# Performance work log

Measured on AMD Instinct MI355X. Metric: run time of the kernel, lower is better.

Reference implementation:

```python
import jax, jax.numpy as jnp
import numpy as np

N_HEAD = 16
HEAD_SIZE = 1024
EMBED = 1024
MULTI_HEAD_SIZE = HEAD_SIZE // N_HEAD  # 64; used only as the softmax scale (source bug)
B, S = 4, 2048


def setup_inputs() -> dict:
    key = jax.random.key(0)
    k1, k2, k3, k4 = jax.random.split(key, 4)
    x = jax.random.normal(k1, (B, S, EMBED), dtype=jnp.float32)
    w_qkv = jax.random.normal(k2, (3 * HEAD_SIZE, EMBED), dtype=jnp.float32) * 0.02
    w_proj = jax.random.normal(k3, (EMBED, HEAD_SIZE), dtype=jnp.float32) * 0.02
    b_proj = jax.random.normal(k4, (EMBED,), dtype=jnp.float32) * 0.02
    return {"x": x, "w_qkv": w_qkv, "w_proj": w_proj, "b_proj": b_proj}


def reference(x, w_qkv, w_proj, b_proj):
    # Fused QKV projection (Linear, no bias): [B,S,E] @ [E,3H] -> split
    qkv = jnp.einsum("bse,he->bsh", x, w_qkv)  # [B,S,3H]
    q, k, v = jnp.split(qkv, 3, axis=-1)       # each [B,S,H]
    # Source's non-flash path: attention over FULL Head_size dim (not per-head),
    # scaled by sqrt(multi_head_size) -- reproduced faithfully.
    scale = 1.0 / np.sqrt(MULTI_HEAD_SIZE).astype(np.float32)
    scores = jnp.einsum("bqh,bkh->bqk", q, k) * scale  # [B,S,S]
    probs = jax.nn.softmax(scores, axis=-1)            # dropout = identity (eval)
    out = jnp.einsum("bqk,bkh->bqh", probs, v)         # [B,S,H]
    # Faithful scrambling reshape: transpose(1,2).contiguous().view(B,S,H)
    Bn, Sn, H = out.shape
    out = jnp.swapaxes(out, 1, 2).reshape(Bn, Sn, H)
    # Output projection + residual dropout (identity in eval)
    out = jnp.einsum("bsh,eh->bse", out, w_proj) + b_proj
    return out
```

## Files before the change

kernel.cpp:

```cpp
#include <hip/hip_runtime.h>


typedef float f32x4 __attribute__((ext_vector_type(4)));
typedef short bf16x8 __attribute__((ext_vector_type(8)));
typedef short bf16x4 __attribute__((ext_vector_type(4)));
typedef unsigned short u16;

#define BM 128
#define BN 128
#define BK 32

__device__ inline u16 f2bf(float f) {
  union { float f; unsigned u; } x; x.f = f;
  unsigned r = x.u + 0x7fffu + ((x.u >> 16) & 1u);
  return (u16)(r >> 16);
}

__device__ inline void gload_lds16(const void* g, void* l) {
  __builtin_amdgcn_global_load_lds(
      (const __attribute__((address_space(1))) void*)g,
      (__attribute__((address_space(3))) void*)l, 16, 0, 0);
}

__global__ __launch_bounds__(256) void cvt_kernel(const float* __restrict__ in,
                                                  u16* __restrict__ out, int n8) {
  int i = blockIdx.x * 256 + threadIdx.x;
  if (i >= n8) return;
  f32x4 a = *(const f32x4*)&in[(long)i * 8];
  f32x4 b = *(const f32x4*)&in[(long)i * 8 + 4];
  bf16x8 o;
#pragma unroll
  for (int j = 0; j < 4; ++j) { o[j] = (short)f2bf(a[j]); o[4 + j] = (short)f2bf(b[j]); }
  *(bf16x8*)&out[(long)i * 8] = o;
}

__global__ __launch_bounds__(256) void transpose_v(const u16* __restrict__ qkvb,
                                                   u16* __restrict__ vT) {
  __shared__ u16 tile[64][72];
  const int t = threadIdx.x;
  const long b = blockIdx.z;
  const int k0 = blockIdx.x * 64, h0 = blockIdx.y * 64;
  const u16* v = qkvb + b * 2048 * 3072 + 2048;
#pragma unroll
  for (int i = 0; i < 2; ++i) {
    int s = i * 256 + t; int r = s >> 3, c = (s & 7) * 8;
    bf16x8 val = *(const bf16x8*)&v[(long)(k0 + r) * 3072 + h0 + c];
    *(bf16x8*)&tile[r][c] = val;
  }
  __syncthreads();
  u16* o = vT + b * 1024 * 2048;
#pragma unroll
  for (int i = 0; i < 2; ++i) {
    int s = i * 256 + t; int r = s >> 3, c = (s & 7) * 8;
    bf16x8 val;
#pragma unroll
    for (int j = 0; j < 8; ++j) val[j] = tile[c + j][r];
    *(bf16x8*)&o[(long)(h0 + r) * 2048 + k0 + c] = val;
  }
}

__global__ __launch_bounds__(256) void softmax_k(const float* __restrict__ S,
                                                 u16* __restrict__ P,
                                                 long sS, long sP) {
  const int t = threadIdx.x;
  const float* row = S + (long)blockIdx.z * sS + (long)blockIdx.x * 2048;
  u16* prow = P + (long)blockIdx.z * sP + (long)blockIdx.x * 2048;
  f32x4 v0 = *(const f32x4*)&row[t * 8];
  f32x4 v1 = *(const f32x4*)&row[t * 8 + 4];
  float m = v0[0];
#pragma unroll
  for (int j = 1; j < 4; ++j) m = fmaxf(m, v0[j]);
#pragma unroll
  for (int j = 0; j < 4; ++j) m = fmaxf(m, v1[j]);
#pragma unroll
  for (int o = 32; o; o >>= 1) m = fmaxf(m, __shfl_xor(m, o));
  __shared__ float red[8];
  if ((t & 63) == 0) red[t >> 6] = m;
  __syncthreads();
  m = fmaxf(fmaxf(red[0], red[1]), fmaxf(red[2], red[3]));
  const float C = 0.18033688011112042f;
  float e[8], s = 0.f;
#pragma unroll
  for (int j = 0; j < 4; ++j) { e[j] = exp2f((v0[j] - m) * C); s += e[j]; }
#pragma unroll
  for (int j = 0; j < 4; ++j) { e[4 + j] = exp2f((v1[j] - m) * C); s += e[4 + j]; }
#pragma unroll
  for (int o = 32; o; o >>= 1) s += __shfl_xor(s, o);
  if ((t & 63) == 0) red[4 + (t >> 6)] = s;
  __syncthreads();
  float inv = 1.f / (red[4] + red[5] + red[6] + red[7]);
  bf16x8 ov;
#pragma unroll
  for (int j = 0; j < 8; ++j) ov[j] = (short)f2bf(e[j] * inv);
  *(bf16x8*)&prow[t * 8] = ov;
}

template <int MODE>
__global__ __launch_bounds__(256) void gemm_nt(const u16* __restrict__ A0, int lda, long sAz,
                                               const u16* __restrict__ B0, int ldb, long sBz,
                                               void* __restrict__ C0, int ldc, long sCz,
                                               const float* __restrict__ bias, int K) {
  __shared__ u16 As[2][BM * BK];
  __shared__ u16 Bs[2][BM * BK];
  const int t = threadIdx.x;
  const int lane = t & 63, wv = t >> 6;
  const long row0 = (long)blockIdx.y * BM, col0 = (long)blockIdx.x * BN;
  const u16* A = A0 + (long)blockIdx.z * sAz;
  const u16* B = B0 + (long)blockIdx.z * sBz;

  f32x4 acc[4][4];
#pragma unroll
  for (int m = 0; m < 4; ++m)
#pragma unroll
    for (int n = 0; n < 4; ++n) acc[m][n] = (f32x4){0.f, 0.f, 0.f, 0.f};

  const int wrow = (wv >> 1) * 64, wcol = (wv & 1) * 64;
  const int fr = lane & 15, fk = (lane >> 4) * 8;

  auto stage = [&](int buf, int k0) {
#pragma unroll
    for (int i = 0; i < 2; ++i) {
      int c = i * 256 + wv * 64 + lane;
      int r = c >> 2, sl = c & 3;
      gload_lds16(A + (row0 + r) * lda + k0 + sl * 8, &As[buf][(i * 256 + wv * 64) * 8]);
    }
#pragma unroll
    for (int i = 0; i < 2; ++i) {
      int c = i * 256 + wv * 64 + lane;
      int r = c >> 2, sl = c & 3;
      gload_lds16(B + (col0 + r) * ldb + k0 + sl * 8, &Bs[buf][(i * 256 + wv * 64) * 8]);
    }
  };

  stage(0, 0);
  __syncthreads();
  const int NK = K / BK;
  for (int kt = 0; kt < NK; ++kt) {
    const int cur = kt & 1;
    if (kt + 1 < NK) stage(cur ^ 1, (kt + 1) * BK);
    bf16x8 af[4], bf[4];
#pragma unroll
    for (int m = 0; m < 4; ++m)
      af[m] = *(const bf16x8*)&As[cur][(wrow + m * 16 + fr) * BK + fk];
#pragma unroll
    for (int n = 0; n < 4; ++n)
      bf[n] = *(const bf16x8*)&Bs[cur][(wcol + n * 16 + fr) * BK + fk];
#pragma unroll
    for (int m = 0; m < 4; ++m)
#pragma unroll
      for (int n = 0; n < 4; ++n)
        acc[m][n] = __builtin_amdgcn_mfma_f32_16x16x32_bf16(af[m], bf[n], acc[m][n], 0, 0, 0);
    __syncthreads();
  }

  const int fq = lane >> 4;
#pragma unroll
  for (int m = 0; m < 4; ++m)
#pragma unroll
    for (int n = 0; n < 4; ++n) {
      const long r0 = row0 + wrow + m * 16 + fq * 4;
      const long c = col0 + wcol + n * 16 + fr;
      if (MODE == 0) {
        float* C = (float*)C0 + (long)blockIdx.z * sCz;
#pragma unroll
        for (int j = 0; j < 4; ++j) C[(r0 + j) * ldc + c] = acc[m][n][j];
      } else if (MODE == 1) {
        u16* C = (u16*)C0 + (long)blockIdx.z * sCz;
#pragma unroll
        for (int j = 0; j < 4; ++j) C[(r0 + j) * ldc + c] = f2bf(acc[m][n][j]);
      } else if (MODE == 2) {
        u16* C = (u16*)C0 + (long)blockIdx.z * sCz;
        const int q0 = (int)r0;
        const long dr = 2 * c + (q0 >> 10);
        bf16x4 pk;
#pragma unroll
        for (int j = 0; j < 4; ++j) pk[j] = (short)f2bf(acc[m][n][j]);
        *(bf16x4*)&C[dr * 1024 + (q0 & 1023)] = pk;
      } else {
        float* C = (float*)C0 + (long)blockIdx.z * sCz;
        const float bv = bias[c];
#pragma unroll
        for (int j = 0; j < 4; ++j) C[(r0 + j) * ldc + c] = acc[m][n][j] + bv;
      }
    }
}

extern "C" void kernel_launch(void* const* d_in, const int* in_sizes, int n_in,
                              void* d_out, int out_size, void* d_ws, size_t ws_size,
                              hipStream_t stream) {
  const float* x      = (const float*)d_in[0];
  const float* w_qkv  = (const float*)d_in[1];
  const float* w_proj = (const float*)d_in[2];
  const float* b_proj = (const float*)d_in[3];
  float* out = (float*)d_out;
  char* ws = (char*)d_ws;

  u16*   xb     = (u16*)(ws + 0);
  u16*   wqkvb  = (u16*)(ws + 16777216);
  u16*   wprojb = (u16*)(ws + 23068672);
  u16*   qkvb   = (u16*)(ws + 25165824);
  u16*   vT     = (u16*)(ws + 75497472);
  u16*   out2   = (u16*)(ws + 92274688);
  float* scores = (float*)(ws + 109051904);
  const bool full = ws_size >= 209715200ull;
  u16* probs = (u16*)(ws + (full ? 176160768 : 125829120));

  cvt_kernel<<<4096, 256, 0, stream>>>(x, xb, 1048576);
  cvt_kernel<<<1536, 256, 0, stream>>>(w_qkv, wqkvb, 393216);
  cvt_kernel<<<512, 256, 0, stream>>>(w_proj, wprojb, 131072);

  gemm_nt<1><<<dim3(24, 64, 1), 256, 0, stream>>>(xb, 1024, 0, wqkvb, 1024, 0,
                                                  qkvb, 3072, 0, nullptr, 1024);
  transpose_v<<<dim3(32, 16, 4), 256, 0, stream>>>(qkvb, vT);

  const long sQ = 2048L * 3072;
  if (full) {
    gemm_nt<0><<<dim3(16, 16, 4), 256, 0, stream>>>(qkvb, 3072, sQ, qkvb + 1024, 3072, sQ,
                                                    scores, 2048, 2048L * 2048, nullptr, 1024);
    softmax_k<<<dim3(2048, 1, 4), 256, 0, stream>>>(scores, probs, 2048L * 2048, 2048L * 2048);
    gemm_nt<2><<<dim3(8, 16, 4), 256, 0, stream>>>(probs, 2048, 2048L * 2048, vT, 2048, 2048L * 1024,
                                                   out2, 1024, 2048L * 1024, nullptr, 2048);
  } else {
    for (int b = 0; b < 4; ++b) {
      const u16* qb = qkvb + (long)b * sQ;
      gemm_nt<0><<<dim3(16, 16, 1), 256, 0, stream>>>(qb, 3072, 0, qb + 1024, 3072, 0,
                                                      scores, 2048, 0, nullptr, 1024);
      softmax_k<<<dim3(2048, 1, 1), 256, 0, stream>>>(scores, probs, 0, 0);
      gemm_nt<2><<<dim3(8, 16, 1), 256, 0, stream>>>(probs, 2048, 0, vT + (long)b * 2048 * 1024, 2048, 0,
                                                     out2 + (long)b * 2048 * 1024, 1024, 0, nullptr, 2048);
    }
  }

  gemm_nt<3><<<dim3(8, 64, 1), 256, 0, stream>>>(out2, 1024, 0, wprojb, 1024, 0,
                                                 out, 1024, 0, b_proj, 1024);
}
```

Before: 324.8 us.

## Replace GEMM with 8-wave larger-tile kernel using interleaved staging and setprio

Replaces the 4-wave 128x128 GEMM with an 8-wave kernel whose tiles are 128 or 256 rows by 256 columns. It stages 64-wide K slices as two 32-wide sub-buffers in dynamic LDS and interleaves the global-to-LDS loads with MFMA phases. Explicit vmcnt waits, raw barriers, sched_barrier and s_setprio control the schedule. The aim is more data reuse per tile and better overlap of memory traffic with matrix compute, at the cost of fewer blocks, more LDS per block and hand-tuned wait counts that must match the issued loads.

```diff
diff --git a/kernel.cpp b/kernel.cpp
--- a/kernel.cpp
+++ b/kernel.cpp
@@ -5,10 +5,6 @@
 typedef short bf16x8 __attribute__((ext_vector_type(8)));
 typedef short bf16x4 __attribute__((ext_vector_type(4)));
 typedef unsigned short u16;
-
-#define BM 128
-#define BN 128
-#define BK 32
 
 __device__ inline u16 f2bf(float f) {
   union { float f; unsigned u; } x; x.f = f;
@@ -95,71 +91,100 @@
   *(bf16x8*)&prow[t * 8] = ov;
 }
 
-template <int MODE>
-__global__ __launch_bounds__(256) void gemm_nt(const u16* __restrict__ A0, int lda, long sAz,
-                                               const u16* __restrict__ B0, int ldb, long sBz,
-                                               void* __restrict__ C0, int ldc, long sCz,
-                                               const float* __restrict__ bias, int K) {
-  __shared__ u16 As[2][BM * BK];
-  __shared__ u16 Bs[2][BM * BK];
-  const int t = threadIdx.x;
-  const int lane = t & 63, wv = t >> 6;
-  const long row0 = (long)blockIdx.y * BM, col0 = (long)blockIdx.x * BN;
+template <int MODE, int BMT>
+__global__ __launch_bounds__(512, 2) void gemm8(const u16* __restrict__ A0, int lda, long sAz,
+                                                const u16* __restrict__ B0, int ldb, long sBz,
+                                                void* __restrict__ C0, int ldc, long sCz,
+                                                const float* __restrict__ bias, int K) {
+  constexpr int MF = BMT / 32;
+  constexpr int LA = BMT / 128;
+  extern __shared__ __align__(16) u16 smem[];
+  u16* Ab = smem;
+  u16* Bb = smem + 4 * BMT * 32;
+  const int t = threadIdx.x, lane = t & 63, wv = t >> 6;
+  const int wr = wv >> 2, wc = wv & 3;
+  const int fr = lane & 15, hi = lane >> 4;
+  const long row0 = (long)blockIdx.y * BMT, col0 = (long)blockIdx.x * 256;
   const u16* A = A0 + (long)blockIdx.z * sAz;
   const u16* B = B0 + (long)blockIdx.z * sBz;
 
-  f32x4 acc[4][4];
-#pragma unroll
-  for (int m = 0; m < 4; ++m)
+  f32x4 acc[MF][4];
+#pragma unroll
+  for (int m = 0; m < MF; ++m)
 #pragma unroll
     for (int n = 0; n < 4; ++n) acc[m][n] = (f32x4){0.f, 0.f, 0.f, 0.f};
 
-  const int wrow = (wv >> 1) * 64, wcol = (wv & 1) * 64;
-  const int fr = lane & 15, fk = (lane >> 4) * 8;
-
-  auto stage = [&](int buf, int k0) {
+  auto stageA = [&](int buf, int ks, int k0) {
+#pragma unroll
+    for (int i = 0; i < LA; ++i) {
+      const int l2 = i * 512 + t;
+      const int r = l2 >> 2, ck = l2 & 3;
+      gload_lds16(A + (row0 + r) * (long)lda + k0 + ks * 32 + ck * 8,
+                  Ab + (buf * 2 + ks) * BMT * 32 + (i * 512 + wv * 64) * 8);
+    }
+  };
+  auto stageB = [&](int buf, int ks, int k0) {
 #pragma unroll
     for (int i = 0; i < 2; ++i) {
-      int c = i * 256 + wv * 64 + lane;
-      int r = c >> 2, sl = c & 3;
-      gload_lds16(A + (row0 + r) * lda + k0 + sl * 8, &As[buf][(i * 256 + wv * 64) * 8]);
-    }
-#pragma unroll
-    for (int i = 0; i < 2; ++i) {
-      int c = i * 256 + wv * 64 + lane;
-      int r = c >> 2, sl = c & 3;
-      gload_lds16(B + (col0 + r) * ldb + k0 + sl * 8, &Bs[buf][(i * 256 + wv * 64) * 8]);
-    }
-  };
-
-  stage(0, 0);
-  __syncthreads();
-  const int NK = K / BK;
-  for (int kt = 0; kt < NK; ++kt) {
-    const int cur = kt & 1;
-    if (kt + 1 < NK) stage(cur ^ 1, (kt + 1) * BK);
-    bf16x8 af[4], bf[4];
-#pragma unroll
-    for (int m = 0; m < 4; ++m)
-      af[m] = *(const bf16x8*)&As[cur][(wrow + m * 16 + fr) * BK + fk];
+      const int l2 = i * 512 + t;
+      const int r = l2 >> 2, ck = l2 & 3;
+      gload_lds16(B + (col0 + r) * (long)ldb + k0 + ks * 32 + ck * 8,
+                  Bb + (buf * 2 + ks) * 256 * 32 + (i * 512 + wv * 64) * 8);
+    }
+  };
+
+  bf16x8 bfr[4];
+  auto loadB = [&](int buf, int ks) {
 #pragma unroll
     for (int n = 0; n < 4; ++n)
-      bf[n] = *(const bf16x8*)&Bs[cur][(wcol + n * 16 + fr) * BK + fk];
-#pragma unroll
-    for (int m = 0; m < 4; ++m)
+      bfr[n] = *(const bf16x8*)(Bb + ((buf * 2 + ks) * 256 + wc * 64 + n * 16 + fr) * 32 + hi * 8);
+  };
+  auto phase = [&](int buf, int ks, int mlo) {
+    bf16x8 afr[MF / 2];
+#pragma unroll
+    for (int m = 0; m < MF / 2; ++m)
+      afr[m] = *(const bf16x8*)(Ab + ((buf * 2 + ks) * BMT + wr * (BMT / 2) + (mlo + m) * 16 + fr) * 32 + hi * 8);
+    __builtin_amdgcn_s_setprio(1);
+#pragma unroll
+    for (int m = 0; m < MF / 2; ++m)
 #pragma unroll
       for (int n = 0; n < 4; ++n)
-        acc[m][n] = __builtin_amdgcn_mfma_f32_16x16x32_bf16(af[m], bf[n], acc[m][n], 0, 0, 0);
-    __syncthreads();
-  }
-
-  const int fq = lane >> 4;
-#pragma unroll
-  for (int m = 0; m < 4; ++m)
+        acc[mlo + m][n] = __builtin_amdgcn_mfma_f32_16x16x32_bf16(afr[m], bfr[n], acc[mlo + m][n], 0, 0, 0);
+    __builtin_amdgcn_s_setprio(0);
+  };
+
+  stageA(0, 0, 0); stageB(0, 0, 0); stageA(0, 1, 0); stageB(0, 1, 0);
+  __builtin_amdgcn_sched_barrier(0);
+  asm volatile("s_waitcnt vmcnt(0)" ::: "memory");
+  __builtin_amdgcn_s_barrier();
+  __builtin_amdgcn_sched_barrier(0);
+
+  const int NT = K >> 6;
+  for (int kt = 0; kt < NT; ++kt) {
+    const int c = kt & 1;
+    const int kn = (kt + 1 < NT) ? ((kt + 1) << 6) : 0;
+    stageA(c ^ 1, 0, kn); loadB(c, 0); phase(c, 0, 0);
+    stageB(c ^ 1, 0, kn); phase(c, 0, MF / 2);
+    __builtin_amdgcn_sched_barrier(0);
+    if constexpr (LA == 2) asm volatile("s_waitcnt vmcnt(4)" ::: "memory");
+    else                   asm volatile("s_waitcnt vmcnt(3)" ::: "memory");
+    __builtin_amdgcn_s_barrier();
+    __builtin_amdgcn_sched_barrier(0);
+    stageA(c ^ 1, 1, kn); loadB(c, 1); phase(c, 1, 0);
+    stageB(c ^ 1, 1, kn); phase(c, 1, MF / 2);
+    __builtin_amdgcn_sched_barrier(0);
+    if constexpr (LA == 2) asm volatile("s_waitcnt vmcnt(4)" ::: "memory");
+    else                   asm volatile("s_waitcnt vmcnt(3)" ::: "memory");
+    __builtin_amdgcn_s_barrier();
+    __builtin_amdgcn_sched_barrier(0);
+  }
+
+#pragma unroll
+  for (int m = 0; m < MF; ++m)
 #pragma unroll
     for (int n = 0; n < 4; ++n) {
-      const long r0 = row0 + wrow + m * 16 + fq * 4;
-      const long c = col0 + wcol + n * 16 + fr;
+      const long r0 = row0 + wr * (BMT / 2) + m * 16 + hi * 4;
+      const long c = col0 + wc * 64 + n * 16 + fr;
       if (MODE == 0) {
         float* C = (float*)C0 + (long)blockIdx.z * sCz;
 #pragma unroll
@@ -205,32 +230,39 @@
   const bool full = ws_size >= 209715200ull;
   u16* probs = (u16*)(ws + (full ? 176160768 : 125829120));
 
+  const int LDS256 = (4 * 256 * 32 + 4 * 256 * 32) * 2;
+  const int LDS128 = (4 * 128 * 32 + 4 * 256 * 32) * 2;
+  hipFuncSetAttribute((const void*)gemm8<1, 128>, hipFuncAttributeMaxDynamicSharedMemorySize, LDS128);
+  hipFuncSetAttribute((const void*)gemm8<0, 256>, hipFuncAttributeMaxDynamicSharedMemorySize, LDS256);
+  hipFuncSetAttribute((const void*)gemm8<2, 128>, hipFuncAttributeMaxDynamicSharedMemorySize, LDS128);
+  hipFuncSetAttribute((const void*)gemm8<3, 128>, hipFuncAttributeMaxDynamicSharedMemorySize, LDS128);
+
   cvt_kernel<<<4096, 256, 0, stream>>>(x, xb, 1048576);
   cvt_kernel<<<1536, 256, 0, stream>>>(w_qkv, wqkvb, 393216);
   cvt_kernel<<<512, 256, 0, stream>>>(w_proj, wprojb, 131072);
 
-  gemm_nt<1><<<dim3(24, 64, 1), 256, 0, stream>>>(xb, 1024, 0, wqkvb, 1024, 0,
-                                                  qkvb, 3072, 0, nullptr, 1024);
+  gemm8<1, 128><<<dim3(12, 64, 1), 512, LDS128, stream>>>(xb, 1024, 0, wqkvb, 1024, 0,
+                                                          qkvb, 3072, 0, nullptr, 1024);
   transpose_v<<<dim3(32, 16, 4), 256, 0, stream>>>(qkvb, vT);
 
   const long sQ = 2048L * 3072;
   if (full) {
-    gemm_nt<0><<<dim3(16, 16, 4), 256, 0, stream>>>(qkvb, 3072, sQ, qkvb + 1024, 3072, sQ,
-                                                    scores, 2048, 2048L * 2048, nullptr, 1024);
+    gemm8<0, 256><<<dim3(8, 8, 4), 512, LDS256, stream>>>(qkvb, 3072, sQ, qkvb + 1024, 3072, sQ,
+                                                          scores, 2048, 2048L * 2048, nullptr, 1024);
     softmax_k<<<dim3(2048, 1, 4), 256, 0, stream>>>(scores, probs, 2048L * 2048, 2048L * 2048);
-    gemm_nt<2><<<dim3(8, 16, 4), 256, 0, stream>>>(probs, 2048, 2048L * 2048, vT, 2048, 2048L * 1024,
-                                                   out2, 1024, 2048L * 1024, nullptr, 2048);
+    gemm8<2, 128><<<dim3(4, 16, 4), 512, LDS128, stream>>>(probs, 2048, 2048L * 2048, vT, 2048, 2048L * 1024,
+                                                           out2, 1024, 2048L * 1024, nullptr, 2048);
   } else {
     for (int b = 0; b < 4; ++b) {
       const u16* qb = qkvb + (long)b * sQ;
-      gemm_nt<0><<<dim3(16, 16, 1), 256, 0, stream>>>(qb, 3072, 0, qb + 1024, 3072, 0,
-                                                      scores, 2048, 0, nullptr, 1024);
+      gemm8<0, 256><<<dim3(8, 8, 1), 512, LDS256, stream>>>(qb, 3072, 0, qb + 1024, 3072, 0,
+                                                            scores, 2048, 0, nullptr, 1024);
       softmax_k<<<dim3(2048, 1, 1), 256, 0, stream>>>(scores, probs, 0, 0);
-      gemm_nt<2><<<dim3(8, 16, 1), 256, 0, stream>>>(probs, 2048, 0, vT + (long)b * 2048 * 1024, 2048, 0,
-                                                     out2 + (long)b * 2048 * 1024, 1024, 0, nullptr, 2048);
-    }
-  }
-
-  gemm_nt<3><<<dim3(8, 64, 1), 256, 0, stream>>>(out2, 1024, 0, wprojb, 1024, 0,
-                                                 out, 1024, 0, b_proj, 1024);
-}
+      gemm8<2, 128><<<dim3(4, 16, 1), 512, LDS128, stream>>>(probs, 2048, 0, vT + (long)b * 2048 * 1024, 2048, 0,
+                                                             out2 + (long)b * 2048 * 1024, 1024, 0, nullptr, 2048);
+    }
+  }
+
+  gemm8<3, 128><<<dim3(4, 64, 1), 512, LDS128, stream>>>(out2, 1024, 0, wprojb, 1024, 0,
+                                                         out, 1024, 0, b_proj, 1024);
+}
```

After: 299.2 us. 7.9% less time.
